# Performance work log

Hardware: AMD Instinct MI355X
Metric: run time of the kernel (lower is better)

## Reference

```python
import jax, jax.numpy as jnp
import numpy as np

T, D, M1, M2, K = 8192, 512, 2048, 2048, 1024


def setup_inputs() -> dict:
    key = jax.random.key(0)
    k = jax.random.split(key, 6)
    s1 = 1.0 / np.sqrt(D + M1)   # layer 1 init scale (1/sqrt(M1_in + M2_out))
    s2 = 1.0 / np.sqrt(M1 + M2)  # layer 2 init scale
    return {
        "X": jax.random.normal(k[0], (T, D), jnp.float32),
        # RNN layer 1 (D -> M1)
        "Wx1": jax.random.normal(k[1], (D, M1), jnp.float32) * s1,
        "Wh1": jax.random.normal(k[2], (M1, M1), jnp.float32) * s1,
        "bh1": jnp.zeros((M1,), jnp.float32),
        "h01": jnp.zeros((M1,), jnp.float32),
        # RNN layer 2 (M1 -> M2)
        "Wx2": jax.random.normal(k[3], (M1, M2), jnp.float32) * s2,
        "Wh2": jax.random.normal(k[4], (M2, M2), jnp.float32) * s2,
        "bh2": jnp.zeros((M2,), jnp.float32),
        "h02": jnp.zeros((M2,), jnp.float32),
        # logistic = nn.Linear(M2, K); store weight as (M2, K) so y = h @ Wl + bl
        "Wl": jax.random.normal(k[5], (M2, K), jnp.float32) / np.sqrt(M2),
        "bl": jnp.zeros((K,), jnp.float32),
    }


def rnn_layer(X, Wx, Wh, bh, h0):
    # X: (T, Din) -> out: (T, Dout). hidden_t = relu((X@Wx)_t + hidden_{t-1} @ Wh + bh)
    Xp = X @ Wx  # (T, Dout) dense GEMM, precomputed as in the torch code

    def step(h, x):
        h = jax.nn.relu(x + h @ Wh + bh)
        return h, h

    _, out = jax.lax.scan(step, h0, Xp)
    return out


def reference(X, Wx1, Wh1, bh1, h01, Wx2, Wh2, bh2, h02, Wl, bl):
    h = rnn_layer(X, Wx1, Wh1, bh1, h01)
    h = rnn_layer(h, Wx2, Wh2, bh2, h02)
    return h @ Wl + bl  # (T, K) logits
```

## Files before the change

### kernel.cpp

```cpp
#include <hip/hip_runtime.h>
#include <cstdint>
#include <cstddef>

#define TT 8192
#define DD 512
#define MM 2048
#define KK 1024

typedef float f32x4 __attribute__((ext_vector_type(4)));
typedef int   i32x4 __attribute__((ext_vector_type(4)));

__device__ __forceinline__ void coh_load2(const int* p, i32x4& a, i32x4& b) {
  asm volatile("global_load_dwordx4 %0, %2, off sc0 sc1\n\t"
               "global_load_dwordx4 %1, %2, off offset:16 sc0 sc1\n\t"
               "s_waitcnt vmcnt(0)"
               : "=v"(a), "=v"(b) : "v"(p) : "memory");
}
__device__ __forceinline__ void coh_store4(float* p, f32x4 v) {
  asm volatile("global_store_dwordx4 %0, %1, off sc0 sc1" :: "v"(p), "v"(v) : "memory");
}
__device__ __forceinline__ void coh_store4x2(float* p, f32x4 a, f32x4 b) {
  asm volatile("global_store_dwordx4 %0, %1, off sc0 sc1\n\t"
               "global_store_dwordx4 %0, %2, off offset:16 sc0 sc1"
               :: "v"(p), "v"(a), "v"(b) : "memory");
}

__device__ __forceinline__ float scrub(float v) {
  return __int_as_float(__float_as_int(v) & 0x7fffffff);
}
__device__ __forceinline__ unsigned short bf16r(float f) {
  unsigned u = __float_as_uint(f);
  return (unsigned short)((u + 0x7fffu + ((u >> 16) & 1u)) >> 16);
}
__device__ __forceinline__ float bflo(unsigned u) { return __uint_as_float(u << 16); }
__device__ __forceinline__ float bfhi(unsigned u) { return __uint_as_float(u & 0xffff0000u); }

__global__ void __launch_bounds__(256) gemm_bias_f32(
    const float* __restrict__ A, const float* __restrict__ B,
    const float* __restrict__ bias, float* __restrict__ C,
    int M, int N, int K)
{
  __shared__ float As[16][128];
  __shared__ float Bs[16][128];
  const int tid = threadIdx.x;
  const int tx = tid & 15, ty = tid >> 4;
  const int row0 = blockIdx.y * 128, col0 = blockIdx.x * 128;
  const int arow = tid >> 1;
  const int ak0  = (tid & 1) * 8;
  const int brow = tid >> 4;
  const int bcol = (tid & 15) * 8;

  const float* Aptr = A + (size_t)(row0 + arow) * K + ak0;
  const float* Bptr = B + (size_t)brow * N + col0 + bcol;

  float acc[8][8];
  #pragma unroll
  for (int i = 0; i < 8; ++i)
    #pragma unroll
    for (int j = 0; j < 8; ++j) acc[i][j] = 0.f;

  for (int kk = 0; kk < K; kk += 16) {
    float4 a0 = *(const float4*)(Aptr + kk);
    float4 a1 = *(const float4*)(Aptr + kk + 4);
    float4 b0 = *(const float4*)(Bptr + (size_t)kk * N);
    float4 b1 = *(const float4*)(Bptr + (size_t)kk * N + 4);
    __syncthreads();
    As[ak0+0][arow] = a0.x; As[ak0+1][arow] = a0.y;
    As[ak0+2][arow] = a0.z; As[ak0+3][arow] = a0.w;
    As[ak0+4][arow] = a1.x; As[ak0+5][arow] = a1.y;
    As[ak0+6][arow] = a1.z; As[ak0+7][arow] = a1.w;
    *(float4*)&Bs[brow][bcol]     = b0;
    *(float4*)&Bs[brow][bcol + 4] = b1;
    __syncthreads();
    #pragma unroll
    for (int k = 0; k < 16; ++k) {
      float4 av0 = *(float4*)&As[k][ty*8];
      float4 av1 = *(float4*)&As[k][ty*8 + 4];
      float4 bv0 = *(float4*)&Bs[k][tx*4];
      float4 bv1 = *(float4*)&Bs[k][64 + tx*4];
      float ar[8] = {av0.x,av0.y,av0.z,av0.w,av1.x,av1.y,av1.z,av1.w};
      float br[8] = {bv0.x,bv0.y,bv0.z,bv0.w,bv1.x,bv1.y,bv1.z,bv1.w};
      #pragma unroll
      for (int i = 0; i < 8; ++i)
        #pragma unroll
        for (int j = 0; j < 8; ++j)
          acc[i][j] += ar[i] * br[j];
    }
  }

  float4 bi0 = *(const float4*)&bias[col0 + tx*4];
  float4 bi1 = *(const float4*)&bias[col0 + 64 + tx*4];
  #pragma unroll
  for (int i = 0; i < 8; ++i) {
    size_t r = (size_t)(row0 + ty*8 + i) * N;
    float4 o0 = make_float4(acc[i][0]+bi0.x, acc[i][1]+bi0.y, acc[i][2]+bi0.z, acc[i][3]+bi0.w);
    float4 o1 = make_float4(acc[i][4]+bi1.x, acc[i][5]+bi1.y, acc[i][6]+bi1.z, acc[i][7]+bi1.w);
    *(float4*)&C[r + col0 + tx*4]      = o0;
    *(float4*)&C[r + col0 + 64 + tx*4] = o1;
  }
}

__global__ void __launch_bounds__(256, 1) rnn_fused(
    const float* __restrict__ Xp1, float* __restrict__ H1, float* __restrict__ H2,
    const float* __restrict__ Wh1, const float* __restrict__ Wx2,
    const float* __restrict__ Wh2, const float* __restrict__ h01,
    const float* __restrict__ h02, const float* __restrict__ bh2)
{
  __shared__ __align__(16) unsigned char smem[147456];
  const int tid  = threadIdx.x;
  const int lane = tid & 63;
  const int wv   = tid >> 6;

  if (blockIdx.x < 128) {
    const int w = blockIdx.x;
    float* WL  = (float*)smem;
    float* h1s = (float*)(smem + 131072);

    for (int r = 0; r < 8; ++r) {
      const int k = tid + 256*r;
      const float* src = &Wh1[(size_t)k*MM + 16*w];
      #pragma unroll
      for (int c4 = 0; c4 < 4; ++c4) {
        float4 q = *(const float4*)(src + 4*c4);
        WL[(4*c4+0)*2048 + k] = q.x;
        WL[(4*c4+1)*2048 + k] = q.y;
        WL[(4*c4+2)*2048 + k] = q.z;
        WL[(4*c4+3)*2048 + k] = q.w;
      }
    }
    const int cbase = 16*w + 4*wv;
    f32x4 xc = {0.f,0.f,0.f,0.f}, xn = xc;
    if (lane == 0) xc = *(const f32x4*)&Xp1[cbase];
    __syncthreads();

    for (int t = 0; t < TT; ++t) {
      if (t == 0) {
        *(float4*)&h1s[8*tid]     = ((const float4*)h01)[2*tid];
        *(float4*)&h1s[8*tid + 4] = ((const float4*)h01)[2*tid + 1];
      } else {
        const int* src = (const int*)(H1 + (size_t)(t-1)*MM + 8*tid);
        i32x4 a, b;
        for (;;) {
          coh_load2(src, a, b);
          if ((a.x|a.y|a.z|a.w|b.x|b.y|b.z|b.w) >= 0) break;
          __builtin_amdgcn_s_sleep(1);
        }
        *(i32x4*)&h1s[8*tid]     = a;
        *(i32x4*)&h1s[8*tid + 4] = b;
      }
      if (lane == 0 && t + 1 < TT)
        xn = *(const f32x4*)&Xp1[(size_t)(t+1)*MM + cbase];
      __syncthreads();

      float s0=0.f, s1=0.f, s2=0.f, s3=0.f;
      #pragma unroll
      for (int i = 0; i < 8; ++i) {
        const int k0 = 4*lane + 256*i;
        f32x4 h  = *(f32x4*)&h1s[k0];
        f32x4 q0 = *(f32x4*)&WL[(4*wv+0)*2048 + k0];
        f32x4 q1 = *(f32x4*)&WL[(4*wv+1)*2048 + k0];
        f32x4 q2 = *(f32x4*)&WL[(4*wv+2)*2048 + k0];
        f32x4 q3 = *(f32x4*)&WL[(4*wv+3)*2048 + k0];
        s0 += h.x*q0.x + h.y*q0.y + h.z*q0.z + h.w*q0.w;
        s1 += h.x*q1.x + h.y*q1.y + h.z*q1.z + h.w*q1.w;
        s2 += h.x*q2.x + h.y*q2.y + h.z*q2.z + h.w*q2.w;
        s3 += h.x*q3.x + h.y*q3.y + h.z*q3.z + h.w*q3.w;
      }
      #pragma unroll
      for (int off = 32; off; off >>= 1) {
        s0 += __shfl_xor(s0, off); s1 += __shfl_xor(s1, off);
        s2 += __shfl_xor(s2, off); s3 += __shfl_xor(s3, off);
      }
      if (lane == 0) {
        f32x4 y;
        y.x = scrub(fmaxf(xc.x + s0, 0.f));
        y.y = scrub(fmaxf(xc.y + s1, 0.f));
        y.z = scrub(fmaxf(xc.z + s2, 0.f));
        y.w = scrub(fmaxf(xc.w + s3, 0.f));
        coh_store4(H1 + (size_t)t*MM + cbase, y);
        xc = xn;
      }
      __syncthreads();
    }
  } else {
    const int w = blockIdx.x - 128;
    unsigned short* W2p = (unsigned short*)smem;
    float* h1s = (float*)(smem + 131072);
    float* h2s = (float*)(smem + 139264);

    for (int r = 0; r < 16; ++r) {
      const int k = tid + 256*r;
      const float* src = (k < MM) ? &Wx2[(size_t)k*MM + 16*w]
                                  : &Wh2[(size_t)(k-MM)*MM + 16*w];
      #pragma unroll
      for (int c4 = 0; c4 < 4; ++c4) {
        float4 q = *(const float4*)(src + 4*c4);
        const int c = 4*c4;
        W2p[((c+0)>>1)*8192 + 2*k + ((c+0)&1)] = bf16r(q.x);
        W2p[((c+1)>>1)*8192 + 2*k + ((c+1)&1)] = bf16r(q.y);
        W2p[((c+2)>>1)*8192 + 2*k + ((c+2)&1)] = bf16r(q.z);
        W2p[((c+3)>>1)*8192 + 2*k + ((c+3)&1)] = bf16r(q.w);
      }
    }
    const int cbase = 16*w + 4*wv;
    f32x4 bv = {0.f,0.f,0.f,0.f};
    if (lane == 0) bv = *(const f32x4*)&bh2[cbase];
    __syncthreads();

    const int cp0 = 2*wv;

    for (int t = 0; t < TT; ++t) {
      {
        const int* p1 = (const int*)(H1 + (size_t)t*MM + 8*tid);
        i32x4 a, b;
        for (;;) {
          coh_load2(p1, a, b);
          if ((a.x|a.y|a.z|a.w|b.x|b.y|b.z|b.w) >= 0) break;
          __builtin_amdgcn_s_sleep(1);
        }
        *(i32x4*)&h1s[8*tid]     = a;
        *(i32x4*)&h1s[8*tid + 4] = b;
      }
      __syncthreads();

      float s0=0.f, s1=0.f, s2=0.f, s3=0.f;
      #pragma unroll
      for (int i = 0; i < 8; ++i) {
        const int k0 = 4*lane + 256*i;
        f32x4 h = *(f32x4*)&h1s[k0];
        uint4 qa = *(uint4*)&W2p[(cp0+0)*8192 + 2*k0];
        uint4 qb = *(uint4*)&W2p[(cp0+1)*8192 + 2*k0];
        s0 += h.x*bflo(qa.x) + h.y*bflo(qa.y) + h.z*bflo(qa.z) + h.w*bflo(qa.w);
        s1 += h.x*bfhi(qa.x) + h.y*bfhi(qa.y) + h.z*bfhi(qa.z) + h.w*bfhi(qa.w);
        s2 += h.x*bflo(qb.x) + h.y*bflo(qb.y) + h.z*bflo(qb.z) + h.w*bflo(qb.w);
        s3 += h.x*bfhi(qb.x) + h.y*bfhi(qb.y) + h.z*bfhi(qb.z) + h.w*bfhi(qb.w);
      }

      if (t == 0) {
        *(float4*)&h2s[8*tid]     = ((const float4*)h02)[2*tid];
        *(float4*)&h2s[8*tid + 4] = ((const float4*)h02)[2*tid + 1];
      } else {
        const int* p2 = (const int*)(H2 + (size_t)(t-1)*MM + 8*tid);
        i32x4 c, d;
        for (;;) {
          coh_load2(p2, c, d);
          if ((c.x|c.y|c.z|c.w|d.x|d.y|d.z|d.w) >= 0) break;
          __builtin_amdgcn_s_sleep(1);
        }
        *(i32x4*)&h2s[8*tid]     = c;
        *(i32x4*)&h2s[8*tid + 4] = d;
      }
      __syncthreads();

      #pragma unroll
      for (int i = 0; i < 8; ++i) {
        const int k0 = 4*lane + 256*i;
        const int kw = 2048 + k0;
        f32x4 h = *(f32x4*)&h2s[k0];
        uint4 qa = *(uint4*)&W2p[(cp0+0)*8192 + 2*kw];
        uint4 qb = *(uint4*)&W2p[(cp0+1)*8192 + 2*kw];
        s0 += h.x*bflo(qa.x) + h.y*bflo(qa.y) + h.z*bflo(qa.z) + h.w*bflo(qa.w);
        s1 += h.x*bfhi(qa.x) + h.y*bfhi(qa.y) + h.z*bfhi(qa.z) + h.w*bfhi(qa.w);
        s2 += h.x*bflo(qb.x) + h.y*bflo(qb.y) + h.z*bflo(qb.z) + h.w*bflo(qb.w);
        s3 += h.x*bfhi(qb.x) + h.y*bfhi(qb.y) + h.z*bfhi(qb.z) + h.w*bfhi(qb.w);
      }
      #pragma unroll
      for (int off = 32; off; off >>= 1) {
        s0 += __shfl_xor(s0, off); s1 += __shfl_xor(s1, off);
        s2 += __shfl_xor(s2, off); s3 += __shfl_xor(s3, off);
      }
      if (lane == 0) {
        f32x4 y;
        y.x = scrub(fmaxf(s0 + bv.x, 0.f));
        y.y = scrub(fmaxf(s1 + bv.y, 0.f));
        y.z = scrub(fmaxf(s2 + bv.z, 0.f));
        y.w = scrub(fmaxf(s3 + bv.w, 0.f));
        coh_store4(H2 + (size_t)t*MM + cbase, y);
      }
      __syncthreads();
    }
  }
}

__global__ void __launch_bounds__(256, 1) rnn_scan_f32(
    const float* __restrict__ Xp, float* __restrict__ H,
    const float* __restrict__ Wh, const float* __restrict__ h0)
{
  __shared__ float h_s[MM];
  __shared__ float h_out[8];
  const int tid  = threadIdx.x;
  const int wg   = blockIdx.x;
  const int lane = tid & 63;
  const int wv   = tid >> 6;
  const int c0   = wg * 8 + wv * 2;

  float4 w0[8], w1[8];
  #pragma unroll
  for (int i = 0; i < 8; ++i) {
    const int kb = lane*4 + 256*i;
    float2 e0 = *(const float2*)&Wh[(size_t)(kb+0)*MM + c0];
    float2 e1 = *(const float2*)&Wh[(size_t)(kb+1)*MM + c0];
    float2 e2 = *(const float2*)&Wh[(size_t)(kb+2)*MM + c0];
    float2 e3 = *(const float2*)&Wh[(size_t)(kb+3)*MM + c0];
    w0[i] = make_float4(e0.x, e1.x, e2.x, e3.x);
    w1[i] = make_float4(e0.y, e1.y, e2.y, e3.y);
  }

  for (int t = 0; t < TT; ++t) {
    float4 ha, hb;
    if (t == 0) {
      ha = ((const float4*)h0)[tid*2];
      hb = ((const float4*)h0)[tid*2 + 1];
    } else {
      const int* src = (const int*)(H + (size_t)(t-1)*MM + tid*8);
      i32x4 a, b;
      do { coh_load2(src, a, b); }
      while ((a.x | a.y | a.z | a.w | b.x | b.y | b.z | b.w) < 0);
      ha = make_float4(__int_as_float(a.x), __int_as_float(a.y),
                       __int_as_float(a.z), __int_as_float(a.w));
      hb = make_float4(__int_as_float(b.x), __int_as_float(b.y),
                       __int_as_float(b.z), __int_as_float(b.w));
    }
    float xv = 0.f;
    if (lane < 2) xv = Xp[(size_t)t*MM + c0 + lane];
    ((float4*)h_s)[tid*2]     = ha;
    ((float4*)h_s)[tid*2 + 1] = hb;
    __syncthreads();

    float s0 = 0.f, s1 = 0.f;
    #pragma unroll
    for (int i = 0; i < 8; ++i) {
      float4 h4 = *(float4*)&h_s[lane*4 + 256*i];
      s0 += h4.x*w0[i].x + h4.y*w0[i].y + h4.z*w0[i].z + h4.w*w0[i].w;
      s1 += h4.x*w1[i].x + h4.y*w1[i].y + h4.z*w1[i].z + h4.w*w1[i].w;
    }
    #pragma unroll
    for (int off = 32; off; off >>= 1) {
      s0 += __shfl_xor(s0, off);
      s1 += __shfl_xor(s1, off);
    }
    if (lane < 2) {
      float s = (lane == 0) ? s0 : s1;
      h_out[wv*2 + lane] = scrub(fmaxf(xv + s, 0.f));
    }
    __syncthreads();
    if (tid == 0) {
      f32x4 o0 = *(f32x4*)&h_out[0];
      f32x4 o1 = *(f32x4*)&h_out[4];
      coh_store4x2(H + (size_t)t*MM + wg*8, o0, o1);
    }
  }
}

extern "C" void kernel_launch(void* const* d_in, const int* in_sizes, int n_in,
                              void* d_out, int out_size, void* d_ws, size_t ws_size,
                              hipStream_t stream) {
  (void)in_sizes; (void)n_in; (void)out_size;

  const float* X   = (const float*)d_in[0];
  const float* Wx1 = (const float*)d_in[1];
  const float* Wh1 = (const float*)d_in[2];
  const float* bh1 = (const float*)d_in[3];
  const float* h01 = (const float*)d_in[4];
  const float* Wx2 = (const float*)d_in[5];
  const float* Wh2 = (const float*)d_in[6];
  const float* bh2 = (const float*)d_in[7];
  const float* h02 = (const float*)d_in[8];
  const float* Wl  = (const float*)d_in[9];
  const float* bl  = (const float*)d_in[10];
  float* out = (float*)d_out;

  const size_t NBUF = (size_t)TT * MM;
  dim3 blk(256);

  if (ws_size >= 3 * NBUF * sizeof(float)) {
    float* Xp1 = (float*)d_ws;
    float* H1  = Xp1 + NBUF;
    float* H2  = H1 + NBUF;

    (void)hipMemsetAsync(H1, 0xFF, 2 * NBUF * sizeof(float), stream);

    gemm_bias_f32<<<dim3(MM/128, TT/128), blk, 0, stream>>>(X, Wx1, bh1, Xp1, TT, MM, DD);

    {
      const float* xp = Xp1; float* h1 = H1; float* h2 = H2;
      const float* wh1 = Wh1; const float* wx2 = Wx2; const float* wh2 = Wh2;
      const float* h01p = h01; const float* h02p = h02; const float* bh2p = bh2;
      void* args[] = {&xp, &h1, &h2, &wh1, &wx2, &wh2, &h01p, &h02p, &bh2p};
      (void)hipLaunchCooperativeKernel((const void*)rnn_fused, dim3(256), blk, args, 0, stream);
    }

    gemm_bias_f32<<<dim3(KK/128, TT/128), blk, 0, stream>>>(H2, Wl, bl, out, TT, KK, MM);
  } else {
    float* bufA = (float*)d_ws;
    float* bufB = bufA + NBUF;

    (void)hipMemsetAsync(bufB, 0xFF, NBUF * sizeof(float), stream);
    gemm_bias_f32<<<dim3(MM/128, TT/128), blk, 0, stream>>>(X, Wx1, bh1, bufA, TT, MM, DD);
    {
      const float* xp = bufA; float* h = bufB; const float* wh = Wh1; const float* h0p = h01;
      void* args[] = {&xp, &h, &wh, &h0p};
      (void)hipLaunchCooperativeKernel((const void*)rnn_scan_f32, dim3(256), blk, args, 0, stream);
    }
    gemm_bias_f32<<<dim3(MM/128, TT/128), blk, 0, stream>>>(bufB, Wx2, bh2, bufA, TT, MM, MM);
    (void)hipMemsetAsync(bufB, 0xFF, NBUF * sizeof(float), stream);
    {
      const float* xp = bufA; float* h = bufB; const float* wh = Wh2; const float* h0p = h02;
      void* args[] = {&xp, &h, &wh, &h0p};
      (void)hipLaunchCooperativeKernel((const void*)rnn_scan_f32, dim3(256), blk, args, 0, stream);
    }
    gemm_bias_f32<<<dim3(KK/128, TT/128), blk, 0, stream>>>(bufA, Wl, bl, out, TT, KK, MM);
  }
}
```

Measured before the change: 25.80 ms.

## Exchange hidden states between blocks as packed bf16 to halve polling traffic

The fused two-layer RNN kernel now publishes per-step hidden states as packed bf16 pairs in separate exchange buffers, with readiness detected through the bf16 sign bits. Only half the threads poll, and each block writes its slice through a single thread after staging results in shared memory. Layer 2 also writes a plain fp32 copy of its output for the final GEMM. This halves the bytes on the latency-critical cross-block dependency chain, but adds an extra sync and pack step per timestep and rounds the recurrent inputs to bf16, which may affect accuracy.

```diff
diff --git a/kernel.cpp b/kernel.cpp
--- a/kernel.cpp
+++ b/kernel.cpp
@@ -9,17 +9,15 @@
 
 typedef float f32x4 __attribute__((ext_vector_type(4)));
 typedef int   i32x4 __attribute__((ext_vector_type(4)));
-
-__device__ __forceinline__ void coh_load2(const int* p, i32x4& a, i32x4& b) {
+typedef unsigned int uint32;
+
+__device__ __forceinline__ void coh_load32(const uint32* p, i32x4& a, i32x4& b) {
   asm volatile("global_load_dwordx4 %0, %2, off sc0 sc1\n\t"
                "global_load_dwordx4 %1, %2, off offset:16 sc0 sc1\n\t"
                "s_waitcnt vmcnt(0)"
                : "=v"(a), "=v"(b) : "v"(p) : "memory");
 }
-__device__ __forceinline__ void coh_store4(float* p, f32x4 v) {
-  asm volatile("global_store_dwordx4 %0, %1, off sc0 sc1" :: "v"(p), "v"(v) : "memory");
-}
-__device__ __forceinline__ void coh_store4x2(float* p, f32x4 a, f32x4 b) {
+__device__ __forceinline__ void coh_store32(uint32* p, i32x4 a, i32x4 b) {
   asm volatile("global_store_dwordx4 %0, %1, off sc0 sc1\n\t"
                "global_store_dwordx4 %0, %2, off offset:16 sc0 sc1"
                :: "v"(p), "v"(a), "v"(b) : "memory");
@@ -28,12 +26,15 @@
 __device__ __forceinline__ float scrub(float v) {
   return __int_as_float(__float_as_int(v) & 0x7fffffff);
 }
-__device__ __forceinline__ unsigned short bf16r(float f) {
-  unsigned u = __float_as_uint(f);
-  return (unsigned short)((u + 0x7fffu + ((u >> 16) & 1u)) >> 16);
-}
-__device__ __forceinline__ float bflo(unsigned u) { return __uint_as_float(u << 16); }
-__device__ __forceinline__ float bfhi(unsigned u) { return __uint_as_float(u & 0xffff0000u); }
+__device__ __forceinline__ uint32 bf16r(float f) {
+  uint32 u = __float_as_uint(f);
+  return (u + 0x7fffu + ((u >> 16) & 1u)) >> 16;
+}
+__device__ __forceinline__ uint32 pack2(float lo, float hi) {
+  return bf16r(lo) | (bf16r(hi) << 16);
+}
+__device__ __forceinline__ float bflo(uint32 u) { return __uint_as_float(u << 16); }
+__device__ __forceinline__ float bfhi(uint32 u) { return __uint_as_float(u & 0xffff0000u); }
 
 __global__ void __launch_bounds__(256) gemm_bias_f32(
     const float* __restrict__ A, const float* __restrict__ B,
@@ -101,20 +102,22 @@
 }
 
 __global__ void __launch_bounds__(256, 1) rnn_fused(
-    const float* __restrict__ Xp1, float* __restrict__ H1, float* __restrict__ H2,
+    const float* __restrict__ Xp1, uint32* __restrict__ H1b,
+    uint32* __restrict__ H2b, float* __restrict__ H2f,
     const float* __restrict__ Wh1, const float* __restrict__ Wx2,
     const float* __restrict__ Wh2, const float* __restrict__ h01,
     const float* __restrict__ h02, const float* __restrict__ bh2)
 {
-  __shared__ __align__(16) unsigned char smem[147456];
+  __shared__ __align__(16) unsigned char smem[139392];
   const int tid  = threadIdx.x;
   const int lane = tid & 63;
   const int wv   = tid >> 6;
 
   if (blockIdx.x < 128) {
     const int w = blockIdx.x;
-    float* WL  = (float*)smem;
-    float* h1s = (float*)(smem + 131072);
+    float*  WL   = (float*)smem;
+    uint32* h1p  = (uint32*)(smem + 131072);
+    float*  hout = (float*)(smem + 135168);
 
     for (int r = 0; r < 8; ++r) {
       const int k = tid + 256*r;
@@ -134,19 +137,26 @@
     __syncthreads();
 
     for (int t = 0; t < TT; ++t) {
-      if (t == 0) {
-        *(float4*)&h1s[8*tid]     = ((const float4*)h01)[2*tid];
-        *(float4*)&h1s[8*tid + 4] = ((const float4*)h01)[2*tid + 1];
-      } else {
-        const int* src = (const int*)(H1 + (size_t)(t-1)*MM + 8*tid);
-        i32x4 a, b;
-        for (;;) {
-          coh_load2(src, a, b);
-          if ((a.x|a.y|a.z|a.w|b.x|b.y|b.z|b.w) >= 0) break;
-          __builtin_amdgcn_s_sleep(1);
+      if (tid < 128) {
+        const int g = tid;
+        if (t == 0) {
+          uint32 d[8];
+          #pragma unroll
+          for (int j = 0; j < 8; ++j)
+            d[j] = pack2(h01[16*g + 2*j], h01[16*g + 2*j + 1]);
+          *(i32x4*)&h1p[8*g]     = *(i32x4*)&d[0];
+          *(i32x4*)&h1p[8*g + 4] = *(i32x4*)&d[4];
+        } else {
+          const uint32* src = H1b + (size_t)(t-1)*1024 + 8*g;
+          i32x4 a, b;
+          for (;;) {
+            coh_load32(src, a, b);
+            if ((((a.x|a.y|a.z|a.w|b.x|b.y|b.z|b.w) & 0x80008000u)) == 0) break;
+            __builtin_amdgcn_s_sleep(1);
+          }
+          *(i32x4*)&h1p[8*g]     = a;
+          *(i32x4*)&h1p[8*g + 4] = b;
         }
-        *(i32x4*)&h1s[8*tid]     = a;
-        *(i32x4*)&h1s[8*tid + 4] = b;
       }
       if (lane == 0 && t + 1 < TT)
         xn = *(const f32x4*)&Xp1[(size_t)(t+1)*MM + cbase];
@@ -156,7 +166,8 @@
       #pragma unroll
       for (int i = 0; i < 8; ++i) {
         const int k0 = 4*lane + 256*i;
-        f32x4 h  = *(f32x4*)&h1s[k0];
+        uint2 dw = *(uint2*)&h1p[k0 >> 1];
+        f32x4 h = {bflo(dw.x), bfhi(dw.x), bflo(dw.y), bfhi(dw.y)};
         f32x4 q0 = *(f32x4*)&WL[(4*wv+0)*2048 + k0];
         f32x4 q1 = *(f32x4*)&WL[(4*wv+1)*2048 + k0];
         f32x4 q2 = *(f32x4*)&WL[(4*wv+2)*2048 + k0];
@@ -177,16 +188,24 @@
         y.y = scrub(fmaxf(xc.y + s1, 0.f));
         y.z = scrub(fmaxf(xc.z + s2, 0.f));
         y.w = scrub(fmaxf(xc.w + s3, 0.f));
-        coh_store4(H1 + (size_t)t*MM + cbase, y);
+        *(f32x4*)&hout[4*wv] = y;
         xc = xn;
       }
       __syncthreads();
+
+      if (tid == 0) {
+        uint32 d[8];
+        #pragma unroll
+        for (int j = 0; j < 8; ++j) d[j] = pack2(hout[2*j], hout[2*j+1]);
+        coh_store32(H1b + (size_t)t*1024 + 8*w, *(i32x4*)&d[0], *(i32x4*)&d[4]);
+      }
     }
   } else {
     const int w = blockIdx.x - 128;
     unsigned short* W2p = (unsigned short*)smem;
-    float* h1s = (float*)(smem + 131072);
-    float* h2s = (float*)(smem + 139264);
+    uint32* h1p  = (uint32*)(smem + 131072);
+    uint32* h2p  = (uint32*)(smem + 135168);
+    float*  hout = (float*)(smem + 139264);
 
     for (int r = 0; r < 16; ++r) {
       const int k = tid + 256*r;
@@ -196,10 +215,10 @@
       for (int c4 = 0; c4 < 4; ++c4) {
         float4 q = *(const float4*)(src + 4*c4);
         const int c = 4*c4;
-        W2p[((c+0)>>1)*8192 + 2*k + ((c+0)&1)] = bf16r(q.x);
-        W2p[((c+1)>>1)*8192 + 2*k + ((c+1)&1)] = bf16r(q.y);
-        W2p[((c+2)>>1)*8192 + 2*k + ((c+2)&1)] = bf16r(q.z);
-        W2p[((c+3)>>1)*8192 + 2*k + ((c+3)&1)] = bf16r(q.w);
+        W2p[((c+0)>>1)*8192 + 2*k + ((c+0)&1)] = (unsigned short)bf16r(q.x);
+        W2p[((c+1)>>1)*8192 + 2*k + ((c+1)&1)] = (unsigned short)bf16r(q.y);
+        W2p[((c+2)>>1)*8192 + 2*k + ((c+2)&1)] = (unsigned short)bf16r(q.z);
+        W2p[((c+3)>>1)*8192 + 2*k + ((c+3)&1)] = (unsigned short)bf16r(q.w);
       }
     }
     const int cbase = 16*w + 4*wv;
@@ -210,16 +229,17 @@
     const int cp0 = 2*wv;
 
     for (int t = 0; t < TT; ++t) {
-      {
-        const int* p1 = (const int*)(H1 + (size_t)t*MM + 8*tid);
+      if (tid < 128) {
+        const int g = tid;
+        const uint32* p1 = H1b + (size_t)t*1024 + 8*g;
         i32x4 a, b;
         for (;;) {
-          coh_load2(p1, a, b);
-          if ((a.x|a.y|a.z|a.w|b.x|b.y|b.z|b.w) >= 0) break;
+          coh_load32(p1, a, b);
+          if ((((a.x|a.y|a.z|a.w|b.x|b.y|b.z|b.w) & 0x80008000u)) == 0) break;
           __builtin_amdgcn_s_sleep(1);
         }
-        *(i32x4*)&h1s[8*tid]     = a;
-        *(i32x4*)&h1s[8*tid + 4] = b;
+        *(i32x4*)&h1p[8*g]     = a;
+        *(i32x4*)&h1p[8*g + 4] = b;
       }
       __syncthreads();
 
@@ -227,7 +247,8 @@
       #pragma unroll
       for (int i = 0; i < 8; ++i) {
         const int k0 = 4*lane + 256*i;
-        f32x4 h = *(f32x4*)&h1s[k0];
+        uint2 dw = *(uint2*)&h1p[k0 >> 1];
+        f32x4 h = {bflo(dw.x), bfhi(dw.x), bflo(dw.y), bfhi(dw.y)};
         uint4 qa = *(uint4*)&W2p[(cp0+0)*8192 + 2*k0];
         uint4 qb = *(uint4*)&W2p[(cp0+1)*8192 + 2*k0];
         s0 += h.x*bflo(qa.x) + h.y*bflo(qa.y) + h.z*bflo(qa.z) + h.w*bflo(qa.w);
@@ -236,19 +257,26 @@
         s3 += h.x*bfhi(qb.x) + h.y*bfhi(qb.y) + h.z*bfhi(qb.z) + h.w*bfhi(qb.w);
       }
 
-      if (t == 0) {
-        *(float4*)&h2s[8*tid]     = ((const float4*)h02)[2*tid];
-        *(float4*)&h2s[8*tid + 4] = ((const float4*)h02)[2*tid + 1];
-      } else {
-        const int* p2 = (const int*)(H2 + (size_t)(t-1)*MM + 8*tid);
-        i32x4 c, d;
-        for (;;) {
-          coh_load2(p2, c, d);
-          if ((c.x|c.y|c.z|c.w|d.x|d.y|d.z|d.w) >= 0) break;
-          __builtin_amdgcn_s_sleep(1);
+      if (tid < 128) {
+        const int g = tid;
+        if (t == 0) {
+          uint32 d[8];
+          #pragma unroll
+          for (int j = 0; j < 8; ++j)
+            d[j] = pack2(h02[16*g + 2*j], h02[16*g + 2*j + 1]);
+          *(i32x4*)&h2p[8*g]     = *(i32x4*)&d[0];
+          *(i32x4*)&h2p[8*g + 4] = *(i32x4*)&d[4];
+        } else {
+          const uint32* p2 = H2b + (size_t)(t-1)*1024 + 8*g;
+          i32x4 c, d;
+          for (;;) {
+            coh_load32(p2, c, d);
+            if ((((c.x|c.y|c.z|c.w|d.x|d.y|d.z|d.w) & 0x80008000u)) == 0) break;
+            __builtin_amdgcn_s_sleep(1);
+          }
+          *(i32x4*)&h2p[8*g]     = c;
+          *(i32x4*)&h2p[8*g + 4] = d;
         }
-        *(i32x4*)&h2s[8*tid]     = c;
-        *(i32x4*)&h2s[8*tid + 4] = d;
       }
       __syncthreads();
 
@@ -256,7 +284,8 @@
       for (int i = 0; i < 8; ++i) {
         const int k0 = 4*lane + 256*i;
         const int kw = 2048 + k0;
-        f32x4 h = *(f32x4*)&h2s[k0];
+        uint2 dw = *(uint2*)&h2p[k0 >> 1];
+        f32x4 h = {bflo(dw.x), bfhi(dw.x), bflo(dw.y), bfhi(dw.y)};
         uint4 qa = *(uint4*)&W2p[(cp0+0)*8192 + 2*kw];
         uint4 qb = *(uint4*)&W2p[(cp0+1)*8192 + 2*kw];
         s0 += h.x*bflo(qa.x) + h.y*bflo(qa.y) + h.z*bflo(qa.z) + h.w*bflo(qa.w);
@@ -275,13 +304,27 @@
         y.y = scrub(fmaxf(s1 + bv.y, 0.f));
         y.z = scrub(fmaxf(s2 + bv.z, 0.f));
         y.w = scrub(fmaxf(s3 + bv.w, 0.f));
-        coh_store4(H2 + (size_t)t*MM + cbase, y);
+        *(f32x4*)&H2f[(size_t)t*MM + cbase] = y;
+        *(f32x4*)&hout[4*wv] = y;
       }
       __syncthreads();
-    }
-  }
-}
-
+
+      if (tid == 0) {
+        uint32 d[8];
+        #pragma unroll
+        for (int j = 0; j < 8; ++j) d[j] = pack2(hout[2*j], hout[2*j+1]);
+        coh_store32(H2b + (size_t)t*1024 + 8*w, *(i32x4*)&d[0], *(i32x4*)&d[4]);
+      }
+    }
+  }
+}
+
+__device__ __forceinline__ void coh_load2f(const int* p, i32x4& a, i32x4& b) {
+  asm volatile("global_load_dwordx4 %0, %2, off sc0 sc1\n\t"
+               "global_load_dwordx4 %1, %2, off offset:16 sc0 sc1\n\t"
+               "s_waitcnt vmcnt(0)"
+               : "=v"(a), "=v"(b) : "v"(p) : "memory");
+}
 __global__ void __launch_bounds__(256, 1) rnn_scan_f32(
     const float* __restrict__ Xp, float* __restrict__ H,
     const float* __restrict__ Wh, const float* __restrict__ h0)
@@ -314,7 +357,7 @@
     } else {
       const int* src = (const int*)(H + (size_t)(t-1)*MM + tid*8);
       i32x4 a, b;
-      do { coh_load2(src, a, b); }
+      do { coh_load2f(src, a, b); }
       while ((a.x | a.y | a.z | a.w | b.x | b.y | b.z | b.w) < 0);
       ha = make_float4(__int_as_float(a.x), __int_as_float(a.y),
                        __int_as_float(a.z), __int_as_float(a.w));
@@ -345,9 +388,9 @@
     }
     __syncthreads();
     if (tid == 0) {
-      f32x4 o0 = *(f32x4*)&h_out[0];
-      f32x4 o1 = *(f32x4*)&h_out[4];
-      coh_store4x2(H + (size_t)t*MM + wg*8, o0, o1);
+      i32x4 o0 = *(i32x4*)&h_out[0];
+      i32x4 o1 = *(i32x4*)&h_out[4];
+      coh_store32((uint32*)(H + (size_t)t*MM + wg*8), o0, o1);
     }
   }
 }
@@ -374,23 +417,24 @@
   dim3 blk(256);
 
   if (ws_size >= 3 * NBUF * sizeof(float)) {
-    float* Xp1 = (float*)d_ws;
-    float* H1  = Xp1 + NBUF;
-    float* H2  = H1 + NBUF;
-
-    (void)hipMemsetAsync(H1, 0xFF, 2 * NBUF * sizeof(float), stream);
+    float*  Xp1 = (float*)d_ws;
+    float*  H2f = Xp1 + NBUF;
+    uint32* H1b = (uint32*)(H2f + NBUF);
+    uint32* H2b = H1b + (size_t)TT * 1024;
+
+    (void)hipMemsetAsync(H1b, 0xFF, 2 * (size_t)TT * 1024 * sizeof(uint32), stream);
 
     gemm_bias_f32<<<dim3(MM/128, TT/128), blk, 0, stream>>>(X, Wx1, bh1, Xp1, TT, MM, DD);
 
     {
-      const float* xp = Xp1; float* h1 = H1; float* h2 = H2;
+      const float* xp = Xp1; uint32* h1b = H1b; uint32* h2b = H2b; float* h2f = H2f;
       const float* wh1 = Wh1; const float* wx2 = Wx2; const float* wh2 = Wh2;
       const float* h01p = h01; const float* h02p = h02; const float* bh2p = bh2;
-      void* args[] = {&xp, &h1, &h2, &wh1, &wx2, &wh2, &h01p, &h02p, &bh2p};
+      void* args[] = {&xp, &h1b, &h2b, &h2f, &wh1, &wx2, &wh2, &h01p, &h02p, &bh2p};
       (void)hipLaunchCooperativeKernel((const void*)rnn_fused, dim3(256), blk, args, 0, stream);
     }
 
-    gemm_bias_f32<<<dim3(KK/128, TT/128), blk, 0, stream>>>(H2, Wl, bl, out, TT, KK, MM);
+    gemm_bias_f32<<<dim3(KK/128, TT/128), blk, 0, stream>>>(H2f, Wl, bl, out, TT, KK, MM);
   } else {
     float* bufA = (float*)d_ws;
     float* bufB = bufA + NBUF;
```

New measurement: 24.13 ms. -6.5%, faster.
